# Kernel optimization log

Hardware: AMD Instinct MI355X
Metric: run time of the kernel (lower is better)

## Reference

```python
import jax, jax.numpy as jnp
import numpy as np

D = 512      # d_model
H = 8        # n_head
L = 6        # n_layers
DFF = 2048   # d_inner
V = 10000    # vocab
NPOS = 2048
B, T = 8, 1023
S = 1024     # encoder length


def sinusoid_table(n_position, d_hid):
    pos = np.arange(n_position)[:, None].astype(np.float64)
    i = np.arange(d_hid)[None, :]
    angle = pos / np.power(10000.0, 2 * (i // 2) / d_hid)
    tab = np.zeros((n_position, d_hid))
    tab[:, 0::2] = np.sin(angle[:, 0::2])
    tab[:, 1::2] = np.cos(angle[:, 1::2])
    return jnp.asarray(tab, jnp.float32)


def layer_norm(x, g, b, eps=1e-6):
    m = x.mean(-1, keepdims=True)
    v = x.var(-1, keepdims=True)
    return (x - m) / jnp.sqrt(v + eps) * g + b


def mha(x, kv, wq, wk, wv, wo, g, b, mask):
    # x: [B,Lq,D], kv: [B,Lk,D], mask: [B,Lq|1,Lk] int or None
    Bq, Lq, _ = x.shape
    Lk = kv.shape[1]
    dk = D // H
    q = (x @ wq).reshape(Bq, Lq, H, dk).transpose(0, 2, 1, 3)   # bhqd
    k = (kv @ wk).reshape(Bq, Lk, H, dk).transpose(0, 2, 1, 3)  # bhkd
    v = (kv @ wv).reshape(Bq, Lk, H, dk).transpose(0, 2, 1, 3)
    scores = jnp.einsum('bhqd,bhkd->bhqk', q, k) / jnp.sqrt(jnp.asarray(dk, x.dtype))
    if mask is not None:
        scores = jnp.where(mask[:, None, :, :] == 0, jnp.asarray(-1e9, x.dtype), scores)
    a = jax.nn.softmax(scores, axis=-1)
    o = jnp.einsum('bhqk,bhkd->bhqd', a, v).transpose(0, 2, 1, 3).reshape(Bq, Lq, D)
    o = o @ wo + x  # residual
    return layer_norm(o, g, b)


def ffn(x, w1, b1, w2, b2, g, b):
    h = jax.nn.relu(x @ w1 + b1)
    return layer_norm(h @ w2 + b2 + x, g, b)


def setup_inputs() -> dict:
    key = jax.random.key(0)
    ks = iter(jax.random.split(key, 64))
    sc = 0.02
    inp = {}
    inp['trg_seq'] = jax.random.randint(next(ks), (B, T), 0, V, dtype=jnp.int32)
    # causal mask over decoder length T+1 (1 = attend)
    T1 = T + 1
    inp['trg_mask'] = jnp.tril(jnp.ones((T1, T1), jnp.int32))[None].repeat(B, axis=0)
    inp['enc_output'] = jax.random.normal(next(ks), (B, S, D), jnp.float32)
    inp['src_mask'] = jnp.ones((B, 1, S), jnp.int32)
    inp['emb'] = jax.random.normal(next(ks), (V, D), jnp.float32) * sc
    inp['ln0_g'] = jnp.ones((D,), jnp.float32)
    inp['ln0_b'] = jnp.zeros((D,), jnp.float32)
    for nm in ['wq_s', 'wk_s', 'wv_s', 'wo_s', 'wq_c', 'wk_c', 'wv_c', 'wo_c']:
        inp[nm] = jax.random.normal(next(ks), (L, D, D), jnp.float32) * sc
    for nm in ['ln1_g', 'ln2_g', 'ln3_g']:
        inp[nm] = jnp.ones((L, D), jnp.float32)
    for nm in ['ln1_b', 'ln2_b', 'ln3_b']:
        inp[nm] = jnp.zeros((L, D), jnp.float32)
    inp['w1'] = jax.random.normal(next(ks), (L, D, DFF), jnp.float32) * sc
    inp['b1'] = jnp.zeros((L, DFF), jnp.float32)
    inp['w2'] = jax.random.normal(next(ks), (L, DFF, D), jnp.float32) * sc
    inp['b2'] = jnp.zeros((L, D), jnp.float32)
    return inp


def reference(trg_seq, trg_mask, enc_output, src_mask, emb, ln0_g, ln0_b,
              wq_s, wk_s, wv_s, wo_s, ln1_g, ln1_b,
              wq_c, wk_c, wv_c, wo_c, ln2_g, ln2_b,
              w1, b1, w2, b2, ln3_g, ln3_b):
    Bq, Tq = trg_seq.shape
    tok = emb[trg_seq]                                         # [B,T,D]
    x = jnp.concatenate([jnp.zeros((Bq, 1, D), tok.dtype), tok], axis=1)  # [B,T+1,D]
    x = x + sinusoid_table(NPOS, D)[None, :Tq + 1]
    x = layer_norm(x, ln0_g, ln0_b)
    for l in range(L):
        x = mha(x, x, wq_s[l], wk_s[l], wv_s[l], wo_s[l], ln1_g[l], ln1_b[l], trg_mask)
        x = mha(x, enc_output, wq_c[l], wk_c[l], wv_c[l], wo_c[l], ln2_g[l], ln2_b[l], src_mask)
        x = ffn(x, w1[l], b1[l], w2[l], b2[l], ln3_g[l], ln3_b[l])
    return x
```

## Files before the change

kernel.cpp:

```cpp
#include <hip/hip_runtime.h>
#include <stdint.h>


typedef unsigned short u16;
typedef float floatx4 __attribute__((ext_vector_type(4)));
typedef short short8 __attribute__((ext_vector_type(8)));

__device__ __forceinline__ float b2f(u16 u) {
    union { unsigned int i; float f; } c; c.i = ((unsigned int)u) << 16; return c.f;
}
__device__ __forceinline__ u16 f2b(float f) {
    union { float f; unsigned int i; } c; c.f = f;
    return (u16)((c.i + 0x7FFFu + ((c.i >> 16) & 1u)) >> 16);
}
__device__ __forceinline__ float ldf(const void* p, size_t i, bool is32) {
    return is32 ? ((const float*)p)[i] : b2f(((const u16*)p)[i]);
}
__device__ __forceinline__ void async16(u16* lds, const u16* g) {
    __builtin_amdgcn_global_load_lds(
        (const __attribute__((address_space(1))) unsigned int*)g,
        (__attribute__((address_space(3))) unsigned int*)lds, 16, 0, 0);
}
__device__ __forceinline__ void xcd_remap(int gx, int gy, int& bx, int& by) {
    const int fid = bx + gx * by;
    const int xcd = fid & 7;
    const int i = fid >> 3;
    bx = i % gx;
    by = xcd * (gy >> 3) + i / gx;
}

__global__ __launch_bounds__(256)
void conv_bf16_kernel(const void* __restrict__ src, u16* __restrict__ dst,
                      const u16* __restrict__ probe)
{
    const bool is32 = (probe[0] == 0);
    const size_t off = ((size_t)blockIdx.x * 256 + threadIdx.x) * 4;
    u16 o[4];
    if (is32) {
        float4 f = *(const float4*)((const float*)src + off);
        o[0] = f2b(f.x); o[1] = f2b(f.y); o[2] = f2b(f.z); o[3] = f2b(f.w);
    } else {
        uint2 vv = *(const uint2*)((const u16*)src + off);
        const u16* pv = (const u16*)&vv;
        o[0] = pv[0]; o[1] = pv[1]; o[2] = pv[2]; o[3] = pv[3];
    }
    *(uint2*)&dst[off] = *(uint2*)o;
}

__global__ __launch_bounds__(256)
void transpose_layer_kernel(const void* __restrict__ wq_s, const void* __restrict__ wk_s,
                            const void* __restrict__ wv_s, const void* __restrict__ wo_s,
                            const void* __restrict__ wq_c, const void* __restrict__ wk_c,
                            const void* __restrict__ wv_c, const void* __restrict__ wo_c,
                            const void* __restrict__ w1,   const void* __restrict__ w2,
                            u16* __restrict__ wT, const u16* __restrict__ probe,
                            size_t loff2, size_t loff1)
{
    __shared__ u16 tile[32][33];
    const bool is32 = (probe[0] == 0);
    const int bid = blockIdx.x;
    const int tid = threadIdx.x;
    const void* src; u16* dst; int C, R, tr, tc; size_t loff;
    if (bid < 2048) {
        const int mat = bid >> 8, t = bid & 255;
        R = 512; C = 512; tr = t >> 4; tc = t & 15; loff = loff2;
        const void* tbl[8] = {wq_s, wk_s, wv_s, wo_s, wq_c, wk_c, wv_c, wo_c};
        src = tbl[mat]; dst = wT + (size_t)mat * 262144;
    } else if (bid < 3072) {
        const int t = bid - 2048;
        R = 512; C = 2048; tr = t >> 6; tc = t & 63; loff = loff1;
        src = w1; dst = wT + 2097152;
    } else {
        const int t = bid - 3072;
        R = 2048; C = 512; tr = t >> 4; tc = t & 15; loff = loff1;
        src = w2; dst = wT + 3145728;
    }
    const int r = tid >> 3, c0 = (tid & 7) * 4;
    const size_t off = loff + (size_t)(tr * 32 + r) * C + tc * 32 + c0;
    u16 vals[4];
    if (is32) {
        float4 f = *(const float4*)((const float*)src + off);
        vals[0] = f2b(f.x); vals[1] = f2b(f.y); vals[2] = f2b(f.z); vals[3] = f2b(f.w);
    } else {
        uint2 vv = *(const uint2*)((const u16*)src + off);
        const u16* pv = (const u16*)&vv;
        vals[0] = pv[0]; vals[1] = pv[1]; vals[2] = pv[2]; vals[3] = pv[3];
    }
#pragma unroll
    for (int j = 0; j < 4; j++) tile[r][c0 + j] = vals[j];
    __syncthreads();
    uint2 ov; u16* po = (u16*)&ov;
#pragma unroll
    for (int j = 0; j < 4; j++) po[j] = tile[c0 + j][r];
    *(uint2*)&dst[(size_t)(tc * 32 + r) * R + tr * 32 + c0] = ov;
}

template<int EPI>
__global__ __launch_bounds__(512)
void gemm256(const u16* __restrict__ A, const u16* __restrict__ Bt,
             const void* __restrict__ bias, size_t boff,
             u16* __restrict__ outb, u16* __restrict__ out1, u16* __restrict__ out2,
             const u16* __restrict__ probe, int M, int N, int K)
{
    __shared__ u16 As[2][256 * 64];
    __shared__ u16 Bs[2][256 * 64];
    const int tid = threadIdx.x;
    const int lane = tid & 63;
    const int quad = lane >> 4, cl = lane & 15;
    const int wave = tid >> 6;
    const int wm2 = (wave >> 2) * 128;
    const int wn2 = (wave & 3) * 64;
    int bx = blockIdx.x, by = blockIdx.y;
    xcd_remap(gridDim.x, gridDim.y, bx, by);
    const int m0 = by * 256, n0 = bx * 256;

    floatx4 acc[8][4];
#pragma unroll
    for (int i = 0; i < 8; i++)
#pragma unroll
        for (int j = 0; j < 4; j++)
#pragma unroll
            for (int r = 0; r < 4; r++) acc[i][j][r] = 0.0f;

    const int lrow = lane >> 3;
    const int lcol = ((lane & 7) ^ lrow) * 8;
    const u16* gA = &A [(size_t)(m0 + wave * 8 + lrow) * K + lcol];
    const u16* gB = &Bt[(size_t)(n0 + wave * 8 + lrow) * K + lcol];

    auto stage = [&](int bsel, int k0) {
#pragma unroll
        for (int s = 0; s < 4; s++)
            async16(&As[bsel][(s * 64 + wave * 8) * 64], gA + (size_t)s * 64 * K + k0);
#pragma unroll
        for (int s = 0; s < 4; s++)
            async16(&Bs[bsel][(s * 64 + wave * 8) * 64], gB + (size_t)s * 64 * K + k0);
    };

    const int nkt = K >> 6;
    stage(0, 0);
    stage(1, 64);

    const int c7 = cl & 7;
    for (int t = 0; t < nkt; ++t) {
        const int cur = t & 1;
        if (t == nkt - 1) asm volatile("s_waitcnt vmcnt(0)" ::: "memory");
        else              asm volatile("s_waitcnt vmcnt(8)" ::: "memory");
        __builtin_amdgcn_sched_barrier(0);
        __builtin_amdgcn_s_barrier();

        const u16* Ac = As[cur];
        const u16* Bc = Bs[cur];
#pragma unroll
        for (int kk = 0; kk < 2; kk++) {
            const int gsw = ((kk * 4 + quad) ^ c7) * 8;
            short8 af[8], bf[4];
#pragma unroll
            for (int mi = 0; mi < 8; mi++)
                af[mi] = *(const short8*)&Ac[(wm2 + mi * 16 + cl) * 64 + gsw];
#pragma unroll
            for (int ni = 0; ni < 4; ni++)
                bf[ni] = *(const short8*)&Bc[(wn2 + ni * 16 + cl) * 64 + gsw];
#pragma unroll
            for (int mi = 0; mi < 8; mi++)
#pragma unroll
                for (int ni = 0; ni < 4; ni++)
                    acc[mi][ni] = __builtin_amdgcn_mfma_f32_16x16x32_bf16(af[mi], bf[ni], acc[mi][ni], 0, 0, 0);
        }
        __builtin_amdgcn_s_barrier();
        __builtin_amdgcn_sched_barrier(0);
        if (t + 2 < nkt) stage(cur, (t + 2) * 64);
    }

    const bool is32 = (probe[0] == 0);
#pragma unroll
    for (int mi = 0; mi < 8; mi++) {
#pragma unroll
        for (int ni = 0; ni < 4; ni++) {
            const int col = n0 + wn2 + ni * 16 + cl;
            const float bv = ldf(bias, boff + col, is32);
#pragma unroll
            for (int r = 0; r < 4; r++) {
                const int row = m0 + wm2 + mi * 16 + quad * 4 + r;
                float v = acc[mi][ni][r] + bv;
                v = fmaxf(v, 0.0f);
                outb[(size_t)row * N + col] = f2b(v);
            }
        }
    }
}

template<int EPI>
__global__ __launch_bounds__(256)
void gemm_bf16(const u16* __restrict__ A, const u16* __restrict__ Bt,
               const void* __restrict__ bias, size_t boff, float* __restrict__ resid,
               u16* __restrict__ outb, u16* __restrict__ out1, u16* __restrict__ out2,
               const u16* __restrict__ probe, int M, int N, int K)
{
    __shared__ u16 As[3][128 * 32];
    __shared__ u16 Bs[3][128 * 32];
    const int tid = threadIdx.x;
    const int lane = tid & 63;
    const int quad = lane >> 4, cl = lane & 15;
    const int wave = tid >> 6;
    const int wm = (wave >> 1) * 64, wn = (wave & 1) * 64;
    int bx = blockIdx.x, by = blockIdx.y;
    xcd_remap(gridDim.x, gridDim.y, bx, by);
    const int m0 = by * 128, n0 = bx * 128;

    const u16* Ause = A;
    if (EPI == 4) {
        const u16* A2 = (const u16*)bias;
        if (A2 != nullptr && n0 >= 512) Ause = A2;
    }

    floatx4 acc[4][4];
#pragma unroll
    for (int i = 0; i < 4; i++)
#pragma unroll
        for (int j = 0; j < 4; j++)
#pragma unroll
            for (int r = 0; r < 4; r++) acc[i][j][r] = 0.0f;

    const int srow = tid >> 2;
    const int scol = (((tid & 3) ^ ((srow >> 1) & 3))) * 8;
    const int rslot = (quad ^ ((cl >> 1) & 3)) * 8;
    const int Ksub = K / gridDim.z;
    const int kbeg = blockIdx.z * Ksub, kend = kbeg + Ksub;
    const int nsteps = (kend - kbeg) >> 5;

    const u16* ga0 = &Ause[(size_t)(m0 + srow) * K + scol];
    const u16* ga1 = &Ause[(size_t)(m0 + 64 + srow) * K + scol];
    const u16* gb0 = &Bt[(size_t)(n0 + srow) * K + scol];
    const u16* gb1 = &Bt[(size_t)(n0 + 64 + srow) * K + scol];

    auto stage = [&](int bsel, int kk) {
        async16(&As[bsel][wave * 512],        ga0 + kk);
        async16(&As[bsel][2048 + wave * 512], ga1 + kk);
        async16(&Bs[bsel][wave * 512],        gb0 + kk);
        async16(&Bs[bsel][2048 + wave * 512], gb1 + kk);
    };

    stage(0, kbeg);
    if (nsteps > 1) stage(1, kbeg + 32);

    for (int t = 0; t < nsteps; ++t) {
        const int cur = t % 3;
        if (t + 2 < nsteps) stage((t + 2) % 3, kbeg + (t + 2) * 32);
        const int rem = nsteps - 1 - t;
        if (rem >= 2)      asm volatile("s_waitcnt vmcnt(8)" ::: "memory");
        else if (rem == 1) asm volatile("s_waitcnt vmcnt(4)" ::: "memory");
        else               asm volatile("s_waitcnt vmcnt(0)" ::: "memory");
        __builtin_amdgcn_sched_barrier(0);
        __builtin_amdgcn_s_barrier();

        const u16* Ac = As[cur];
        const u16* Bc = Bs[cur];
        short8 af[4], bfr[4];
#pragma unroll
        for (int mi = 0; mi < 4; mi++) af[mi]  = *(const short8*)&Ac[(wm + mi * 16 + cl) * 32 + rslot];
#pragma unroll
        for (int ni = 0; ni < 4; ni++) bfr[ni] = *(const short8*)&Bc[(wn + ni * 16 + cl) * 32 + rslot];
#pragma unroll
        for (int mi = 0; mi < 4; mi++)
#pragma unroll
            for (int ni = 0; ni < 4; ni++)
                acc[mi][ni] = __builtin_amdgcn_mfma_f32_16x16x32_bf16(af[mi], bfr[ni], acc[mi][ni], 0, 0, 0);
        __builtin_amdgcn_s_barrier();
    }

    if (EPI == 4) {
        const int seg = n0 >> 9;
        const int cbase = (n0 & 511) + wn;
        if (seg < 2) {
            u16* dst = (seg == 0) ? outb : out1;
#pragma unroll
            for (int mi = 0; mi < 4; mi++)
#pragma unroll
                for (int ni = 0; ni < 4; ni++) {
                    const int c = cbase + ni * 16 + cl;
#pragma unroll
                    for (int r = 0; r < 4; r++)
                        dst[(size_t)(m0 + wm + mi * 16 + quad * 4 + r) * 512 + c] = f2b(acc[mi][ni][r]);
                }
        } else {
            u16* dst = out2;
#pragma unroll
            for (int mi = 0; mi < 4; mi++) {
                const int row0 = m0 + wm + mi * 16 + quad * 4;
                const int b8 = (row0 >> 10) * 8;
                const int key0 = row0 & 1023;
#pragma unroll
                for (int ni = 0; ni < 4; ni++) {
                    const int c = cbase + ni * 16 + cl;
                    u16 pk[4];
#pragma unroll
                    for (int r = 0; r < 4; r++) pk[r] = f2b(acc[mi][ni][r]);
                    const size_t vrow = (size_t)(b8 + (c >> 6)) * 64 + (c & 63);
                    *(uint2*)&dst[vrow * 1024 + key0] = *(uint2*)pk;
                }
            }
        }
        return;
    }

    bool is32 = false;
    if (EPI == 1 || EPI == 2 || EPI == 3) is32 = (probe[0] == 0);
    const bool addbias = (bias != nullptr) && (blockIdx.z == 0);
    float* pslice = (EPI == 3) ? resid + (size_t)blockIdx.z * M * N : resid;
#pragma unroll
    for (int mi = 0; mi < 4; mi++) {
#pragma unroll
        for (int ni = 0; ni < 4; ni++) {
            const int col = n0 + wn + ni * 16 + cl;
#pragma unroll
            for (int r = 0; r < 4; r++) {
                const int row = m0 + wm + mi * 16 + quad * 4 + r;
                float v = acc[mi][ni][r];
                if (EPI == 1) { v += ldf(bias, boff + col, is32); v = fmaxf(v, 0.0f); }
                if (EPI == 2) {
                    if (addbias) v += ldf(bias, boff + col, is32);
                    atomicAdd(&resid[(size_t)row * N + col], v);
                } else if (EPI == 3) {
                    if (addbias) v += ldf(bias, boff + col, is32);
                    pslice[(size_t)row * N + col] = v;
                } else {
                    outb[(size_t)row * N + col] = f2b(v);
                }
            }
        }
    }
}

template<int CAUSAL>
__global__ __launch_bounds__(256)
void attn_kernel(const u16* __restrict__ Q, const u16* __restrict__ Kb,
                 const u16* __restrict__ VT, u16* __restrict__ O)
{
    __shared__ u16 Kt[64][72];
    __shared__ u16 Vt[64][72];
    int qt = blockIdx.x, bh = blockIdx.y;
    xcd_remap(gridDim.x, gridDim.y, qt, bh);
    const int b = bh >> 3, h = bh & 7;
    const int tid = threadIdx.x;
    const int w = tid >> 6;
    const int lane = tid & 63;
    const int quad = lane >> 4, cl = lane & 15;

    const size_t qrow = (size_t)(b * 1024 + qt * 64 + w * 16 + cl) * 512 + h * 64;
    const short8 qf0 = *(const short8*)&Q[qrow + quad * 8];
    const short8 qf1 = *(const short8*)&Q[qrow + 32 + quad * 8];
    const int qg = qt * 64 + w * 16 + cl;

    float lsum = 0.0f;
    floatx4 oacc[4];
#pragma unroll
    for (int nb = 0; nb < 4; nb++)
#pragma unroll
        for (int r = 0; r < 4; r++) oacc[nb][r] = 0.0f;

    const int trow = tid >> 3, tcol = (tid & 7) * 8;
    const int tv = tid & 7;
    const int vm = (tv >> 2) * 32 + (tv & 1) * 16 + ((tv >> 1) & 1) * 4;
    const size_t kbase = (size_t)(b * 1024) * 512 + h * 64;
    const size_t vbase = (size_t)(bh * 64) * 1024;

    const int nkt = CAUSAL ? (qt + 1) : 16;
    uint4 ka0 = *(const uint4*)&Kb[kbase + (size_t)trow * 512 + tcol];
    uint4 ka1 = *(const uint4*)&Kb[kbase + (size_t)(trow + 32) * 512 + tcol];
    uint4 va0 = *(const uint4*)&VT[vbase + (size_t)trow * 1024 + tcol];
    uint4 va1 = *(const uint4*)&VT[vbase + (size_t)(trow + 32) * 1024 + tcol];

    for (int kt = 0; kt < nkt; kt++) {
        *(uint4*)&Kt[trow][tcol]      = ka0;
        *(uint4*)&Kt[trow + 32][tcol] = ka1;
        *(uint2*)&Vt[trow][vm]          = make_uint2(va0.x, va0.y);
        *(uint2*)&Vt[trow][vm + 8]      = make_uint2(va0.z, va0.w);
        *(uint2*)&Vt[trow + 32][vm]     = make_uint2(va1.x, va1.y);
        *(uint2*)&Vt[trow + 32][vm + 8] = make_uint2(va1.z, va1.w);
        if (kt + 1 < nkt) {
            const int k1 = (kt + 1) * 64;
            ka0 = *(const uint4*)&Kb[kbase + (size_t)(k1 + trow) * 512 + tcol];
            ka1 = *(const uint4*)&Kb[kbase + (size_t)(k1 + trow + 32) * 512 + tcol];
            va0 = *(const uint4*)&VT[vbase + (size_t)trow * 1024 + k1 + tcol];
            va1 = *(const uint4*)&VT[vbase + (size_t)(trow + 32) * 1024 + k1 + tcol];
        }
        asm volatile("s_waitcnt lgkmcnt(0)" ::: "memory");
        __builtin_amdgcn_sched_barrier(0);
        __builtin_amdgcn_s_barrier();
        __builtin_amdgcn_sched_barrier(0);

        const int k0 = kt * 64;
        floatx4 sacc[4];
#pragma unroll
        for (int kb2 = 0; kb2 < 4; kb2++)
#pragma unroll
            for (int r = 0; r < 4; r++) sacc[kb2][r] = 0.0f;
#pragma unroll
        for (int kb2 = 0; kb2 < 4; kb2++) {
            const short8 kf0 = *(const short8*)&Kt[kb2 * 16 + cl][quad * 8];
            const short8 kf1 = *(const short8*)&Kt[kb2 * 16 + cl][32 + quad * 8];
            sacc[kb2] = __builtin_amdgcn_mfma_f32_16x16x32_bf16(kf0, qf0, sacc[kb2], 0, 0, 0);
            sacc[kb2] = __builtin_amdgcn_mfma_f32_16x16x32_bf16(kf1, qf1, sacc[kb2], 0, 0, 0);
        }
        const bool need_mask = CAUSAL && (kt == nkt - 1);
        float p[4][4];
#pragma unroll
        for (int kb2 = 0; kb2 < 4; kb2++) {
#pragma unroll
            for (int r = 0; r < 4; r++) {
                float e = __expf(sacc[kb2][r] * 0.125f);
                if (need_mask) {
                    const int key = k0 + kb2 * 16 + quad * 4 + r;
                    e = (key > qg) ? 0.0f : e;
                }
                p[kb2][r] = e;
                lsum += e;
            }
        }
        unsigned int pk[4][2];
#pragma unroll
        for (int kb2 = 0; kb2 < 4; kb2++) {
            asm("v_cvt_pk_bf16_f32 %0, %1, %2" : "=v"(pk[kb2][0]) : "v"(p[kb2][0]), "v"(p[kb2][1]));
            asm("v_cvt_pk_bf16_f32 %0, %1, %2" : "=v"(pk[kb2][1]) : "v"(p[kb2][2]), "v"(p[kb2][3]));
        }
#pragma unroll
        for (int c = 0; c < 2; c++) {
            union { short8 s8; unsigned int u[4]; } pa;
            pa.u[0] = pk[2 * c][0];     pa.u[1] = pk[2 * c][1];
            pa.u[2] = pk[2 * c + 1][0]; pa.u[3] = pk[2 * c + 1][1];
#pragma unroll
            for (int nb = 0; nb < 4; nb++) {
                const short8 vf = *(const short8*)&Vt[nb * 16 + cl][c * 32 + quad * 8];
                oacc[nb] = __builtin_amdgcn_mfma_f32_16x16x32_bf16(pa.s8, vf, oacc[nb], 0, 0, 0);
            }
        }
        __builtin_amdgcn_sched_barrier(0);
        __builtin_amdgcn_s_barrier();
        __builtin_amdgcn_sched_barrier(0);
    }
    lsum += __shfl_xor(lsum, 16, 64);
    lsum += __shfl_xor(lsum, 32, 64);
    float inv[4];
#pragma unroll
    for (int r = 0; r < 4; r++) inv[r] = 1.0f / __shfl(lsum, quad * 4 + r, 64);
#pragma unroll
    for (int nb = 0; nb < 4; nb++) {
#pragma unroll
        for (int r = 0; r < 4; r++) {
            const float v = oacc[nb][r] * inv[r];
            O[(size_t)(b * 1024 + qt * 64 + w * 16 + quad * 4 + r) * 512 + h * 64 + nb * 16 + cl] = f2b(v);
        }
    }
}

__device__ __forceinline__ float2 block_ln_512(float v0, float v1,
                                               float g0, float g1, float b0, float b1,
                                               int tid)
{
    __shared__ float red[8];
    float s = v0 + v1, sq = v0 * v0 + v1 * v1;
#pragma unroll
    for (int m = 1; m < 64; m <<= 1) { s += __shfl_xor(s, m, 64); sq += __shfl_xor(sq, m, 64); }
    const int wv = tid >> 6;
    if ((tid & 63) == 0) { red[wv * 2] = s; red[wv * 2 + 1] = sq; }
    __syncthreads();
    s  = red[0] + red[2] + red[4] + red[6];
    sq = red[1] + red[3] + red[5] + red[7];
    const float mean = s * (1.0f / 512.0f);
    const float var = sq * (1.0f / 512.0f) - mean * mean;
    const float rstd = rsqrtf(var + 1e-6f);
    return make_float2((v0 - mean) * rstd * g0 + b0, (v1 - mean) * rstd * g1 + b1);
}

__global__ __launch_bounds__(256)
void ln_kernel(float* __restrict__ xf, const void* __restrict__ g, const void* __restrict__ bb,
               size_t goff, const u16* __restrict__ probe,
               u16* __restrict__ xb, void* __restrict__ finalout,
               const float* __restrict__ p0, const float* __restrict__ p1)
{
    const bool is32 = (probe[0] == 0);
    const int row = blockIdx.x, tid = threadIdx.x;
    const int i = tid * 2;
    const size_t base = (size_t)row * 512;
    float2 v = *(const float2*)&xf[base + i];
    if (p0) {
        const float2 a = *(const float2*)&p0[base + i];
        v.x += a.x; v.y += a.y;
    }
    if (p1) {
        const float2 b = *(const float2*)&p1[base + i];
        v.x += b.x; v.y += b.y;
    }
    const float2 y = block_ln_512(v.x, v.y, ldf(g, goff + i, is32), ldf(g, goff + i + 1, is32),
                                  ldf(bb, goff + i, is32), ldf(bb, goff + i + 1, is32), tid);
    if (finalout) {
        if (is32) {
            *(float2*)&((float*)finalout)[base + i] = y;
        } else {
            u16* ob = (u16*)finalout;
            ob[base + i] = f2b(y.x); ob[base + i + 1] = f2b(y.y);
        }
    } else {
        *(float2*)&xf[base + i] = y;
        xb[base + i] = f2b(y.x); xb[base + i + 1] = f2b(y.y);
    }
}

__global__ __launch_bounds__(256)
void embed_ln_kernel(const int* __restrict__ trg_seq, const void* __restrict__ emb,
                     const void* __restrict__ g, const void* __restrict__ bb,
                     const u16* __restrict__ probe,
                     float* __restrict__ xf, u16* __restrict__ xb)
{
    const bool is32 = (probe[0] == 0);
    const int row = blockIdx.x;
    const int b = row >> 10, t = row & 1023;
    const int tid = threadIdx.x;
    const int tok = (t == 0) ? -1 : trg_seq[b * 1023 + t - 1];
    const int i = tid * 2;
    const float freq = __expf((float)i * (-9.210340371976184f / 512.0f));
    const float angle = (float)t * freq;
    float v0 = sinf(angle), v1 = cosf(angle);
    if (tok >= 0) {
        v0 += ldf(emb, (size_t)tok * 512 + i, is32);
        v1 += ldf(emb, (size_t)tok * 512 + i + 1, is32);
    }
    const float2 y = block_ln_512(v0, v1, ldf(g, i, is32), ldf(g, i + 1, is32),
                                  ldf(bb, i, is32), ldf(bb, i + 1, is32), tid);
    const size_t base = (size_t)row * 512;
    *(float2*)&xf[base + i] = y;
    xb[base + i] = f2b(y.x); xb[base + i + 1] = f2b(y.y);
}

extern "C" void kernel_launch(void* const* d_in, const int* in_sizes, int n_in,
                              void* d_out, int out_size, void* d_ws, size_t ws_size,
                              hipStream_t stream)
{
    const int* trg_seq = (const int*)d_in[0];
    const void* enc   = d_in[2];
    const void* emb   = d_in[4];
    const void* ln0_g = d_in[5];
    const void* ln0_b = d_in[6];
    const u16* probe  = (const u16*)d_in[5];

    char* ws = (char*)d_ws;
    float* xf   = (float*)(ws);
    u16*   xb   = (u16*)  (ws + (16u << 20));
    u16*   qb   = (u16*)  (ws + (24u << 20));
    u16*   kb   = (u16*)  (ws + (32u << 20));
    u16*   vt   = (u16*)  (ws + (40u << 20));
    u16*   ao   = (u16*)  (ws + (48u << 20));
    u16*   hb   = (u16*)  (ws + (24u << 20));
    u16*   wT   = (u16*)  (ws + (56u << 20));
    u16*   encb = (u16*)  (ws + (64u << 20));
    const bool bigws = ws_size >= (108ull << 20);
    float* p0 = (float*)(ws + (72u << 20));
    float* p1 = (float*)(ws + (88u << 20));
    const float* lp0 = bigws ? p0 : nullptr;
    const float* lp1 = bigws ? p1 : nullptr;

    const size_t E2 = 262144, E1 = 1048576;
    const dim3 gqkv(12, 64);
    const dim3 gffn1(8, 32);
    const dim3 gproj(4, 64);
    const dim3 gffn2(4, 64, 2), gattn(16, 64);

    conv_bf16_kernel<<<4096, 256, 0, stream>>>(enc, encb, probe);
    embed_ln_kernel<<<8192, 256, 0, stream>>>(trg_seq, emb, ln0_g, ln0_b, probe, xf, xb);

    for (int l = 0; l < 6; l++) {
        transpose_layer_kernel<<<4096, 256, 0, stream>>>(
            d_in[7], d_in[8], d_in[9], d_in[10], d_in[11], d_in[12], d_in[13], d_in[14],
            d_in[21], d_in[23], wT, probe, (size_t)l * E2, (size_t)l * E1);

        gemm_bf16<4><<<gqkv, 256, 0, stream>>>(xb, wT, xb, 0, nullptr,
                                               qb, kb, vt, probe, 8192, 1536, 512);
        attn_kernel<1><<<gattn, 256, 0, stream>>>(qb, kb, vt, ao);
        if (bigws)
            gemm_bf16<3><<<gproj, 256, 0, stream>>>(ao, wT + 3 * E2, nullptr, 0, p0,
                                                    nullptr, nullptr, nullptr, probe, 8192, 512, 512);
        else
            gemm_bf16<2><<<gproj, 256, 0, stream>>>(ao, wT + 3 * E2, nullptr, 0, xf,
                                                    nullptr, nullptr, nullptr, probe, 8192, 512, 512);
        ln_kernel<<<8192, 256, 0, stream>>>(xf, d_in[15], d_in[18], (size_t)l * 512, probe, xb,
                                            nullptr, lp0, nullptr);

        gemm_bf16<4><<<gqkv, 256, 0, stream>>>(xb, wT + 4 * E2, encb, 0, nullptr,
                                               qb, kb, vt, probe, 8192, 1536, 512);
        attn_kernel<0><<<gattn, 256, 0, stream>>>(qb, kb, vt, ao);
        if (bigws)
            gemm_bf16<3><<<gproj, 256, 0, stream>>>(ao, wT + 7 * E2, nullptr, 0, p0,
                                                    nullptr, nullptr, nullptr, probe, 8192, 512, 512);
        else
            gemm_bf16<2><<<gproj, 256, 0, stream>>>(ao, wT + 7 * E2, nullptr, 0, xf,
                                                    nullptr, nullptr, nullptr, probe, 8192, 512, 512);
        ln_kernel<<<8192, 256, 0, stream>>>(xf, d_in[16], d_in[19], (size_t)l * 512, probe, xb,
                                            nullptr, lp0, nullptr);

        gemm256<1><<<gffn1, 512, 0, stream>>>(xb, wT + 2097152, d_in[22], (size_t)l * 2048,
                                              hb, nullptr, nullptr, probe, 8192, 2048, 512);
        if (bigws)
            gemm_bf16<3><<<gffn2, 256, 0, stream>>>(hb, wT + 3145728, d_in[24], (size_t)l * 512, p0,
                                                    nullptr, nullptr, nullptr, probe, 8192, 512, 2048);
        else
            gemm_bf16<2><<<gffn2, 256, 0, stream>>>(hb, wT + 3145728, d_in[24], (size_t)l * 512, xf,
                                                    nullptr, nullptr, nullptr, probe, 8192, 512, 2048);
        ln_kernel<<<8192, 256, 0, stream>>>(xf, d_in[17], d_in[20], (size_t)l * 512, probe, xb,
                                            (l == 5) ? d_out : nullptr, lp0, lp1);
    }
}
```

Measured before the change: 1.637 ms.

## Widen attention blocks to 128 queries with double-buffered K/V tiles

The attention kernel now runs 512 threads (8 waves) per block covering 128 query rows, so each staged 64-key K/V tile is shared by twice as many queries and global K/V traffic per query halves. The K/V LDS tiles are double-buffered, which allows dropping the trailing barrier in each key-tile iteration, leaving one barrier per step. For causal attention the block now walks 2*qt+2 key tiles and masks the last two. The lower-half waves therefore do a fully masked extra tile, and the larger blocks reduce the block count and may lower occupancy.

```diff
diff --git a/kernel.cpp b/kernel.cpp
--- a/kernel.cpp
+++ b/kernel.cpp
@@ -332,12 +332,12 @@
 }
 
 template<int CAUSAL>
-__global__ __launch_bounds__(256)
+__global__ __launch_bounds__(512)
 void attn_kernel(const u16* __restrict__ Q, const u16* __restrict__ Kb,
                  const u16* __restrict__ VT, u16* __restrict__ O)
 {
-    __shared__ u16 Kt[64][72];
-    __shared__ u16 Vt[64][72];
+    __shared__ u16 Kt[2][64][72];
+    __shared__ u16 Vt[2][64][72];
     int qt = blockIdx.x, bh = blockIdx.y;
     xcd_remap(gridDim.x, gridDim.y, qt, bh);
     const int b = bh >> 3, h = bh & 7;
@@ -346,10 +346,10 @@
     const int lane = tid & 63;
     const int quad = lane >> 4, cl = lane & 15;
 
-    const size_t qrow = (size_t)(b * 1024 + qt * 64 + w * 16 + cl) * 512 + h * 64;
+    const size_t qrow = (size_t)(b * 1024 + qt * 128 + w * 16 + cl) * 512 + h * 64;
     const short8 qf0 = *(const short8*)&Q[qrow + quad * 8];
     const short8 qf1 = *(const short8*)&Q[qrow + 32 + quad * 8];
-    const int qg = qt * 64 + w * 16 + cl;
+    const int qg = qt * 128 + w * 16 + cl;
 
     float lsum = 0.0f;
     floatx4 oacc[4];
@@ -364,25 +364,20 @@
     const size_t kbase = (size_t)(b * 1024) * 512 + h * 64;
     const size_t vbase = (size_t)(bh * 64) * 1024;
 
-    const int nkt = CAUSAL ? (qt + 1) : 16;
-    uint4 ka0 = *(const uint4*)&Kb[kbase + (size_t)trow * 512 + tcol];
-    uint4 ka1 = *(const uint4*)&Kb[kbase + (size_t)(trow + 32) * 512 + tcol];
-    uint4 va0 = *(const uint4*)&VT[vbase + (size_t)trow * 1024 + tcol];
-    uint4 va1 = *(const uint4*)&VT[vbase + (size_t)(trow + 32) * 1024 + tcol];
+    const int nkt = CAUSAL ? (2 * qt + 2) : 16;
+    uint4 ka = *(const uint4*)&Kb[kbase + (size_t)trow * 512 + tcol];
+    uint4 va = *(const uint4*)&VT[vbase + (size_t)trow * 1024 + tcol];
 
     for (int kt = 0; kt < nkt; kt++) {
-        *(uint4*)&Kt[trow][tcol]      = ka0;
-        *(uint4*)&Kt[trow + 32][tcol] = ka1;
-        *(uint2*)&Vt[trow][vm]          = make_uint2(va0.x, va0.y);
-        *(uint2*)&Vt[trow][vm + 8]      = make_uint2(va0.z, va0.w);
-        *(uint2*)&Vt[trow + 32][vm]     = make_uint2(va1.x, va1.y);
-        *(uint2*)&Vt[trow + 32][vm + 8] = make_uint2(va1.z, va1.w);
+        const int cur = kt & 1;
+        asm volatile("s_waitcnt vmcnt(0)" ::: "memory");
+        *(uint4*)&Kt[cur][trow][tcol]      = ka;
+        *(uint2*)&Vt[cur][trow][vm]        = make_uint2(va.x, va.y);
+        *(uint2*)&Vt[cur][trow][vm + 8]    = make_uint2(va.z, va.w);
         if (kt + 1 < nkt) {
             const int k1 = (kt + 1) * 64;
-            ka0 = *(const uint4*)&Kb[kbase + (size_t)(k1 + trow) * 512 + tcol];
-            ka1 = *(const uint4*)&Kb[kbase + (size_t)(k1 + trow + 32) * 512 + tcol];
-            va0 = *(const uint4*)&VT[vbase + (size_t)trow * 1024 + k1 + tcol];
-            va1 = *(const uint4*)&VT[vbase + (size_t)(trow + 32) * 1024 + k1 + tcol];
+            ka = *(const uint4*)&Kb[kbase + (size_t)(k1 + trow) * 512 + tcol];
+            va = *(const uint4*)&VT[vbase + (size_t)trow * 1024 + k1 + tcol];
         }
         asm volatile("s_waitcnt lgkmcnt(0)" ::: "memory");
         __builtin_amdgcn_sched_barrier(0);
@@ -397,12 +392,12 @@
             for (int r = 0; r < 4; r++) sacc[kb2][r] = 0.0f;
 #pragma unroll
         for (int kb2 = 0; kb2 < 4; kb2++) {
-            const short8 kf0 = *(const short8*)&Kt[kb2 * 16 + cl][quad * 8];
-            const short8 kf1 = *(const short8*)&Kt[kb2 * 16 + cl][32 + quad * 8];
+            const short8 kf0 = *(const short8*)&Kt[cur][kb2 * 16 + cl][quad * 8];
+            const short8 kf1 = *(const short8*)&Kt[cur][kb2 * 16 + cl][32 + quad * 8];
             sacc[kb2] = __builtin_amdgcn_mfma_f32_16x16x32_bf16(kf0, qf0, sacc[kb2], 0, 0, 0);
             sacc[kb2] = __builtin_amdgcn_mfma_f32_16x16x32_bf16(kf1, qf1, sacc[kb2], 0, 0, 0);
         }
-        const bool need_mask = CAUSAL && (kt == nkt - 1);
+        const bool need_mask = CAUSAL && (kt >= nkt - 2);
         float p[4][4];
 #pragma unroll
         for (int kb2 = 0; kb2 < 4; kb2++) {
@@ -430,13 +425,10 @@
             pa.u[2] = pk[2 * c + 1][0]; pa.u[3] = pk[2 * c + 1][1];
 #pragma unroll
             for (int nb = 0; nb < 4; nb++) {
-                const short8 vf = *(const short8*)&Vt[nb * 16 + cl][c * 32 + quad * 8];
+                const short8 vf = *(const short8*)&Vt[cur][nb * 16 + cl][c * 32 + quad * 8];
                 oacc[nb] = __builtin_amdgcn_mfma_f32_16x16x32_bf16(pa.s8, vf, oacc[nb], 0, 0, 0);
             }
         }
-        __builtin_amdgcn_sched_barrier(0);
-        __builtin_amdgcn_s_barrier();
-        __builtin_amdgcn_sched_barrier(0);
     }
     lsum += __shfl_xor(lsum, 16, 64);
     lsum += __shfl_xor(lsum, 32, 64);
@@ -448,7 +440,7 @@
 #pragma unroll
         for (int r = 0; r < 4; r++) {
             const float v = oacc[nb][r] * inv[r];
-            O[(size_t)(b * 1024 + qt * 64 + w * 16 + quad * 4 + r) * 512 + h * 64 + nb * 16 + cl] = f2b(v);
+            O[(size_t)(b * 1024 + qt * 128 + w * 16 + quad * 4 + r) * 512 + h * 64 + nb * 16 + cl] = f2b(v);
         }
     }
 }
@@ -563,7 +555,8 @@
     const dim3 gqkv(12, 64);
     const dim3 gffn1(8, 32);
     const dim3 gproj(4, 64);
-    const dim3 gffn2(4, 64, 2), gattn(16, 64);
+    const dim3 gffn2(4, 64, 2);
+    const dim3 gattn(8, 64);
 
     conv_bf16_kernel<<<4096, 256, 0, stream>>>(enc, encb, probe);
     embed_ln_kernel<<<8192, 256, 0, stream>>>(trg_seq, emb, ln0_g, ln0_b, probe, xf, xb);
@@ -575,7 +568,7 @@
 
         gemm_bf16<4><<<gqkv, 256, 0, stream>>>(xb, wT, xb, 0, nullptr,
                                                qb, kb, vt, probe, 8192, 1536, 512);
-        attn_kernel<1><<<gattn, 256, 0, stream>>>(qb, kb, vt, ao);
+        attn_kernel<1><<<gattn, 512, 0, stream>>>(qb, kb, vt, ao);
         if (bigws)
             gemm_bf16<3><<<gproj, 256, 0, stream>>>(ao, wT + 3 * E2, nullptr, 0, p0,
                                                     nullptr, nullptr, nullptr, probe, 8192, 512, 512);
@@ -587,7 +580,7 @@
 
         gemm_bf16<4><<<gqkv, 256, 0, stream>>>(xb, wT + 4 * E2, encb, 0, nullptr,
                                                qb, kb, vt, probe, 8192, 1536, 512);
-        attn_kernel<0><<<gattn, 256, 0, stream>>>(qb, kb, vt, ao);
+        attn_kernel<0><<<gattn, 512, 0, stream>>>(qb, kb, vt, ao);
         if (bigws)
             gemm_bf16<3><<<gproj, 256, 0, stream>>>(ao, wT + 7 * E2, nullptr, 0, p0,
                                                     nullptr, nullptr, nullptr, probe, 8192, 512, 512);
```

Result: no change. 1.612 ms (-1.6%).
